# Kernel optimization log

Hardware: AMD Instinct MI355X
Metric: run time of the kernel (lower is better)

Reference implementation:

```python
import jax, jax.numpy as jnp
import numpy as np

B, Q, K, D, H, DH = 4, 512, 4096, 1024, 8, 128  # qk_channels=v_channels=out=1024

def setup_inputs() -> dict:
    key = jax.random.key(0)
    ks = jax.random.split(key, 5)
    s = 1.0 / np.sqrt(D)
    return {
        "inputs_q": jax.random.normal(ks[0], (B, Q, D), jnp.float32),
        "inputs_kv": jax.random.normal(ks[1], (B, K, D), jnp.float32),
        "Wq": jax.random.normal(ks[2], (D, H, DH), jnp.float32) * s,
        "Wkv": jax.random.normal(ks[3], (D, H, 2 * DH), jnp.float32) * s,
        "Wproj": jax.random.normal(ks[4], (H, DH, D), jnp.float32) * (1.0 / np.sqrt(H * DH)),
        "b_proj": jnp.zeros((D,), jnp.float32),
    }

def reference(inputs_q, inputs_kv, Wq, Wkv, Wproj, b_proj):
    # QKV projections (no bias)
    q = jnp.einsum('bqd,dhe->bqhe', inputs_q, Wq)          # [B,Q,H,DH]
    kv = jnp.einsum('bkd,dhe->bkhe', inputs_kv, Wkv)        # [B,K,H,2*DH]
    k, v = kv[..., :DH], kv[..., DH:]
    # scaled dot-product attention (softmax in fp32, per source)
    attn = jnp.einsum('bqhd,bkhd->bhqk', q, k) / np.sqrt(DH)
    attn = jax.nn.softmax(attn.astype(jnp.float32), axis=-1).astype(v.dtype)
    o = jnp.einsum('bhqk,bkhd->bqhd', attn, v)              # [B,Q,H,DH]
    # output projection contracting (head, head_dim), with bias
    return jnp.einsum('bqhd,hdo->bqo', o, Wproj) + b_proj   # [B,Q,D]
```

## Files before the change

### kernel.cpp

```cpp
#include <hip/hip_runtime.h>
#include <hip/hip_bf16.h>
#include <cstdint>

typedef unsigned short u16;
typedef unsigned int u32;
typedef __bf16 bf16x8 __attribute__((ext_vector_type(8)));
typedef u16 u16x8 __attribute__((ext_vector_type(8)));
typedef u16 u16x4 __attribute__((ext_vector_type(4)));
typedef float f32x4 __attribute__((ext_vector_type(4)));

#define MFMA16(a, b, c) __builtin_amdgcn_mfma_f32_16x16x32_bf16(a, b, c, 0, 0, 0)

__device__ __forceinline__ void async16(const void* g, void* s) {
    __builtin_amdgcn_global_load_lds((const __attribute__((address_space(1))) void*)g,
                                     (__attribute__((address_space(3))) void*)s, 16, 0, 0);
}

__device__ __forceinline__ u16 f2bf(float f) {
    u32 u; __builtin_memcpy(&u, &f, 4);
    u = u + 0x7fffu + ((u >> 16) & 1u);
    return (u16)(u >> 16);
}

__global__ __launch_bounds__(256) void prep_all(const float* __restrict__ inq,
                                                u16* __restrict__ Aq,
                                                const float* __restrict__ inkv,
                                                u16* __restrict__ Akv,
                                                const float* __restrict__ Wq,  u16* __restrict__ WqT,
                                                const float* __restrict__ Wkv, u16* __restrict__ WkvT,
                                                const float* __restrict__ Wp,  u16* __restrict__ WpT) {
    __shared__ u16 t[64][65];
    const int blk = blockIdx.x;
    const int tid = threadIdx.x;
    if (blk < 9216) {
        const float* in; u16* out; size_t i;
        if (blk < 1024) { in = inq;  out = Aq;  i = (size_t)blk * 256 + tid; }
        else            { in = inkv; out = Akv; i = (size_t)(blk - 1024) * 256 + tid; }
        const float4* p = (const float4*)in + i * 2;
        const float4 a = p[0], b = p[1];
        u16x8 v;
        v[0] = f2bf(a.x); v[1] = f2bf(a.y); v[2] = f2bf(a.z); v[3] = f2bf(a.w);
        v[4] = f2bf(b.x); v[5] = f2bf(b.y); v[6] = f2bf(b.z); v[7] = f2bf(b.w);
        ((u16x8*)out)[i] = v;
        return;
    }
    const int wblk = blk - 9216;
    const float* in; u16* out; int R, C, bx, by;
    if (wblk < 256)      { in = Wq;  out = WqT;  R = 1024; C = 1024; bx = wblk & 15;  by = wblk >> 4; }
    else if (wblk < 768) { in = Wkv; out = WkvT; R = 1024; C = 2048; bx = (wblk - 256) & 31; by = (wblk - 256) >> 5; }
    else                 { in = Wp;  out = WpT;  R = 1024; C = 1024; bx = (wblk - 768) & 15; by = (wblk - 768) >> 4; }
    const int r0 = by << 6, c0 = bx << 6;
#pragma unroll
    for (int i = 0; i < 16; i++) {
        int idx = i * 256 + tid;
        int r = idx >> 6, c = idx & 63;
        t[r][c] = f2bf(in[(size_t)(r0 + r) * C + c0 + c]);
    }
    __syncthreads();
#pragma unroll
    for (int i = 0; i < 16; i++) {
        int idx = i * 256 + tid;
        int c = idx >> 6, r = idx & 63;
        out[(size_t)(c0 + c) * R + r0 + r] = t[r][c];
    }
}

template <bool OUTF32, int NT>
__global__ __launch_bounds__(256) void gemm_bt(const u16* __restrict__ A,
                                               const u16* __restrict__ B,
                                               void* __restrict__ Cv,
                                               const float* __restrict__ bias,
                                               int M, int N, int K) {
    constexpr int NJ = NT / 32;
    __shared__ __align__(16) u16 As[128 * 64];
    __shared__ __align__(16) u16 Bs[NT * 64];
    const int tid = threadIdx.x;
    const int wave = tid >> 6, lane = tid & 63;
    const int lrow = lane & 15, quad = lane >> 4;
    const int nb = N / NT;
    const int bx = blockIdx.x % nb, by = blockIdx.x / nb;
    const long m0 = (long)by << 7, n0 = (long)bx * NT;
    const int wm = (wave >> 1) << 6, wn = (wave & 1) * (NT / 2);

    const f32x4 fz = {0.f, 0.f, 0.f, 0.f};
    f32x4 acc[4][NJ];
#pragma unroll
    for (int i = 0; i < 4; i++)
#pragma unroll
        for (int j = 0; j < NJ; j++) acc[i][j] = fz;

    const int srow = wave * 8 + (lane >> 3);
    const int scol = ((lane & 7) ^ (lane >> 3)) << 3;
    const u16* Ag = A + (m0 + srow) * K + scol;
    const u16* Bg = B + (n0 + srow) * K + scol;
    u16* AsW = &As[wave * 512];
    u16* BsW = &Bs[wave * 512];

    for (int k0 = 0; k0 < K; k0 += 64) {
        __syncthreads();
#pragma unroll
        for (int c = 0; c < 4; c++)
            async16(Ag + (long)c * 32 * K + k0, AsW + c * 2048);
#pragma unroll
        for (int c = 0; c < NT / 32; c++)
            async16(Bg + (long)c * 32 * K + k0, BsW + c * 2048);
        __syncthreads();
#pragma unroll
        for (int c = 0; c < 2; c++) {
            bf16x8 af[4], bfr[NJ];
#pragma unroll
            for (int i = 0; i < 4; i++) {
                const int row = wm + i * 16 + lrow;
                af[i] = *(const bf16x8*)&As[row * 64 + (((c * 4 + quad) ^ (row & 7)) << 3)];
            }
#pragma unroll
            for (int j = 0; j < NJ; j++) {
                const int row = wn + j * 16 + lrow;
                bfr[j] = *(const bf16x8*)&Bs[row * 64 + (((c * 4 + quad) ^ (row & 7)) << 3)];
            }
#pragma unroll
            for (int i = 0; i < 4; i++)
#pragma unroll
                for (int j = 0; j < NJ; j++)
                    acc[i][j] = MFMA16(bfr[j], af[i], acc[i][j]);
        }
    }
#pragma unroll
    for (int i = 0; i < 4; i++) {
        const long row = m0 + wm + i * 16 + lrow;
#pragma unroll
        for (int j = 0; j < NJ; j++) {
            const long colb = n0 + wn + j * 16 + quad * 4;
            if (OUTF32) {
                f32x4 v = acc[i][j];
                if (bias) v += *(const f32x4*)&bias[colb];
                *(f32x4*)&((float*)Cv)[row * N + colb] = v;
            } else {
                u16x4 pk;
#pragma unroll
                for (int r = 0; r < 4; r++) pk[r] = f2bf(acc[i][j][r]);
                *(u16x4*)&((u16*)Cv)[row * N + colb] = pk;
            }
        }
    }
}

__global__ __launch_bounds__(512, 2) void gemm_kv256(const u16* __restrict__ A,
                                                     const u16* __restrict__ B,
                                                     u16* __restrict__ C,
                                                     u16* __restrict__ Vt) {
    constexpr int K = 1024, N = 2048, NT = 16;
    __shared__ __align__(16) u16 As[2][256 * 64];
    __shared__ __align__(16) u16 Bs[2][256 * 64];
    const int tid = threadIdx.x;
    const int wave = tid >> 6, lane = tid & 63;
    const int lrow = lane & 15, quad = lane >> 4;
    const int wMi = wave >> 2, wNi = wave & 3;
    const int wm = wMi * 128, wn = wNi * 64;
    const int wg = blockIdx.x;
    const int swz = (wg & 7) * 64 + (wg >> 3);
    const int bx = swz & 7, by = swz >> 3;
    const long m0 = (long)by << 8, n0 = (long)bx << 8;

    const int srow = tid >> 3;
    const int scol = ((tid & 7) ^ (srow & 7)) << 3;
    const u16* Ag = A + (m0 + srow) * K + scol;
    const u16* Bg = B + (n0 + srow) * K + scol;
    const int sdst = tid * 8;

    auto stgA = [&](int bi, int h, int kt) {
        async16(Ag + (size_t)(h * 128) * K + kt * 64,      &As[bi][h * 8192 + sdst]);
        async16(Ag + (size_t)(h * 128 + 64) * K + kt * 64, &As[bi][h * 8192 + 4096 + sdst]);
    };
    auto stgB = [&](int bi, int h, int kt) {
        async16(Bg + (size_t)(h * 128) * K + kt * 64,      &Bs[bi][h * 8192 + sdst]);
        async16(Bg + (size_t)(h * 128 + 64) * K + kt * 64, &Bs[bi][h * 8192 + 4096 + sdst]);
    };

    stgB(0, 0, 0); stgB(0, 1, 0); stgA(0, 0, 0); stgA(0, 1, 0);
    stgB(1, 0, 1); stgB(1, 1, 1); stgA(1, 0, 1);

    const f32x4 fz = {0.f, 0.f, 0.f, 0.f};
    f32x4 acc[8][4];
#pragma unroll
    for (int i = 0; i < 8; i++)
#pragma unroll
        for (int j = 0; j < 4; j++) acc[i][j] = fz;

    asm volatile("s_waitcnt vmcnt(6)" ::: "memory");
    __builtin_amdgcn_s_barrier();

    bf16x8 av[4][2], bv[4][2];
    for (int t = 0; t < NT; ++t) {
        const int cur = t & 1, nxt = cur ^ 1;
#pragma unroll
        for (int i = 0; i < 4; i++) {
            const int row = wm + i * 16 + lrow;
#pragma unroll
            for (int c = 0; c < 2; c++)
                av[i][c] = *(const bf16x8*)&As[cur][row * 64 + (((c * 4 + quad) ^ (row & 7)) << 3)];
        }
#pragma unroll
        for (int j = 0; j < 4; j++) {
            const int row = wn + j * 16 + lrow;
#pragma unroll
            for (int c = 0; c < 2; c++)
                bv[j][c] = *(const bf16x8*)&Bs[cur][row * 64 + (((c * 4 + quad) ^ (row & 7)) << 3)];
        }
        if (t + 1 < NT) stgA(nxt, 1, t + 1);
        __builtin_amdgcn_s_barrier();
        asm volatile("s_waitcnt lgkmcnt(0)" ::: "memory");
        __builtin_amdgcn_sched_barrier(0);
        __builtin_amdgcn_s_setprio(1);
#pragma unroll
        for (int i = 0; i < 4; i++)
#pragma unroll
            for (int j = 0; j < 2; j++)
#pragma unroll
                for (int c = 0; c < 2; c++)
                    acc[i][j] = MFMA16(av[i][c], bv[j][c], acc[i][j]);
        __builtin_amdgcn_s_setprio(0);
        __builtin_amdgcn_s_barrier();
        if (t + 2 < NT) stgB(cur, 0, t + 2);
        __builtin_amdgcn_s_barrier();
        __builtin_amdgcn_sched_barrier(0);
        __builtin_amdgcn_s_setprio(1);
#pragma unroll
        for (int i = 0; i < 4; i++)
#pragma unroll
            for (int j = 2; j < 4; j++)
#pragma unroll
                for (int c = 0; c < 2; c++)
                    acc[i][j] = MFMA16(av[i][c], bv[j][c], acc[i][j]);
        __builtin_amdgcn_s_setprio(0);
        __builtin_amdgcn_s_barrier();
#pragma unroll
        for (int i = 0; i < 4; i++) {
            const int row = wm + (i + 4) * 16 + lrow;
#pragma unroll
            for (int c = 0; c < 2; c++)
                av[i][c] = *(const bf16x8*)&As[cur][row * 64 + (((c * 4 + quad) ^ (row & 7)) << 3)];
        }
        if (t + 2 < NT) stgB(cur, 1, t + 2);
        __builtin_amdgcn_s_barrier();
        asm volatile("s_waitcnt lgkmcnt(0)" ::: "memory");
        __builtin_amdgcn_sched_barrier(0);
        __builtin_amdgcn_s_setprio(1);
#pragma unroll
        for (int i = 0; i < 4; i++)
#pragma unroll
            for (int j = 0; j < 2; j++)
#pragma unroll
                for (int c = 0; c < 2; c++)
                    acc[i + 4][j] = MFMA16(av[i][c], bv[j][c], acc[i + 4][j]);
        __builtin_amdgcn_s_setprio(0);
        __builtin_amdgcn_s_barrier();
        if (t + 2 < NT) stgA(cur, 0, t + 2);
        __builtin_amdgcn_s_barrier();
        __builtin_amdgcn_sched_barrier(0);
        __builtin_amdgcn_s_setprio(1);
#pragma unroll
        for (int i = 0; i < 4; i++)
#pragma unroll
            for (int j = 2; j < 4; j++)
#pragma unroll
                for (int c = 0; c < 2; c++)
                    acc[i + 4][j] = MFMA16(av[i][c], bv[j][c], acc[i + 4][j]);
        __builtin_amdgcn_s_setprio(0);
        if (t + 2 < NT)      { asm volatile("s_waitcnt vmcnt(6)" ::: "memory"); }
        else if (t + 1 < NT) { asm volatile("s_waitcnt vmcnt(0)" ::: "memory"); }
        __builtin_amdgcn_s_barrier();
    }

    const int h = bx;
    if (wNi < 2) {
#pragma unroll
        for (int j = 0; j < 4; j++) {
            const long col = n0 + wn + j * 16 + lrow;
#pragma unroll
            for (int i = 0; i < 8; i++) {
                const long row = m0 + wm + i * 16 + quad * 4;
#pragma unroll
                for (int r = 0; r < 4; r++)
                    C[(row + r) * N + col] = f2bf(acc[i][j][r]);
            }
        }
    } else {
#pragma unroll
        for (int j = 0; j < 4; j++) {
            const int dh = (wNi - 2) * 64 + j * 16 + lrow;
#pragma unroll
            for (int i = 0; i < 8; i++) {
                const int row = (int)m0 + wm + i * 16 + quad * 4;
                const int b = row >> 12, kv = row & 4095;
                u16x4 pk;
#pragma unroll
                for (int r = 0; r < 4; r++) pk[r] = f2bf(acc[i][j][r]);
                *(u16x4*)&Vt[(((size_t)b * 8 + h) * 128 + dh) * 4096 + kv] = pk;
            }
        }
    }
}

__global__ __launch_bounds__(512, 4) void flash_attn_split(const u16* __restrict__ qb,
                                                           const u16* __restrict__ kvb,
                                                           const u16* __restrict__ vTb,
                                                           float* __restrict__ Opart,
                                                           float* __restrict__ Mpart,
                                                           float* __restrict__ Lpart) {
    __shared__ __align__(16) u16 Ks[2][64 * 128];
    __shared__ __align__(16) u16 Vs[2][128 * 64];
    __shared__ __align__(16) u16 Ps[8][16 * 64];
    const int tid = threadIdx.x, wave = tid >> 6, lane = tid & 63;
    const int lrow = lane & 15, quad = lane >> 4;
    const int p = blockIdx.x;
    const int blk = (p & 7) * 64 + (p >> 3);
    const int split = blk & 3, qt = (blk >> 2) & 3, h = (blk >> 4) & 7, b = blk >> 7;
    const int q0 = qt * 128;
    const int kbase = split * 1024;

    bf16x8 qf[4];
    {
        const u16* qp = qb + (((size_t)(b * 512 + q0 + wave * 16 + lrow) * 8 + h) << 7) + quad * 8;
#pragma unroll
        for (int c = 0; c < 4; c++) qf[c] = *(const bf16x8*)(qp + c * 32);
    }

    const f32x4 fz = {0.f, 0.f, 0.f, 0.f};
    f32x4 oacc[8];
#pragma unroll
    for (int g = 0; g < 8; g++) oacc[g] = fz;
    float mrow = -1e30f, lsum = 0.f;
    const float scale = 0.08838834764831845f;

    const int kRow = tid >> 4, kBlk = tid & 15;
    const int vRow = tid >> 3, vBlk = tid & 7;
    const u16* kg = kvb + (size_t)b * 4096 * 2048 + h * 256 + kBlk * 8;
    const u16* vg = vTb + (size_t)(b * 8 + h) * 128 * 4096 + vBlk * 8;
    const int ksw = (kBlk ^ (kRow & 15)) << 3;
    const int vsw = (vBlk ^ (vRow & 7)) << 3;

    {
        const bf16x8 a0 = *(const bf16x8*)&kg[(size_t)(kbase + kRow) * 2048];
        const bf16x8 a1 = *(const bf16x8*)&kg[(size_t)(kbase + 32 + kRow) * 2048];
        const bf16x8 b0 = *(const bf16x8*)&vg[(size_t)vRow * 4096 + kbase];
        const bf16x8 b1 = *(const bf16x8*)&vg[(size_t)(64 + vRow) * 4096 + kbase];
        *(bf16x8*)&Ks[0][kRow * 128 + ksw] = a0;
        *(bf16x8*)&Ks[0][(32 + kRow) * 128 + ksw] = a1;
        *(bf16x8*)&Vs[0][vRow * 64 + vsw] = b0;
        *(bf16x8*)&Vs[0][(64 + vRow) * 64 + vsw] = b1;
    }
    __syncthreads();

    for (int it = 0; it < 16; ++it) {
        const int cur = it & 1, nxt = cur ^ 1;
        const bool more = (it + 1 < 16);
        bf16x8 nk0, nk1, nv0, nv1;
        if (more) {
            const int k1 = kbase + (it + 1) * 64;
            nk0 = *(const bf16x8*)&kg[(size_t)(k1 + kRow) * 2048];
            nk1 = *(const bf16x8*)&kg[(size_t)(k1 + 32 + kRow) * 2048];
            nv0 = *(const bf16x8*)&vg[(size_t)vRow * 4096 + k1];
            nv1 = *(const bf16x8*)&vg[(size_t)(64 + vRow) * 4096 + k1];
        }

        f32x4 s[4];
        __builtin_amdgcn_s_setprio(1);
#pragma unroll
        for (int t = 0; t < 4; t++) {
            f32x4 a = fz;
#pragma unroll
            for (int c = 0; c < 4; c++) {
                const bf16x8 kf = *(const bf16x8*)
                    &Ks[cur][(t * 16 + lrow) * 128 + (((c * 4 + quad) ^ lrow) << 3)];
                a = MFMA16(kf, qf[c], a);
            }
            s[t] = a * scale;
        }
        __builtin_amdgcn_s_setprio(0);

        float mx = s[0][0];
#pragma unroll
        for (int t = 0; t < 4; t++)
#pragma unroll
            for (int r = 0; r < 4; r++) mx = fmaxf(mx, s[t][r]);
        mx = fmaxf(mx, __shfl_xor(mx, 16));
        mx = fmaxf(mx, __shfl_xor(mx, 32));
        float mn = fmaxf(mrow, mx);
        if (__all(mx <= mrow + 8.f)) {
            mn = mrow;
        } else {
            const float alpha = __expf(mrow - mn);
#pragma unroll
            for (int g = 0; g < 8; g++) oacc[g] *= alpha;
            lsum *= alpha;
            mrow = mn;
        }
        float sum = 0.f;
#pragma unroll
        for (int t = 0; t < 4; t++)
#pragma unroll
            for (int r = 0; r < 4; r++) {
                float pv = __expf(s[t][r] - mn);
                s[t][r] = pv;
                sum += pv;
            }
        sum += __shfl_xor(sum, 16);
        sum += __shfl_xor(sum, 32);
        lsum += sum;

        u16* Pw = &Ps[wave][0];
#pragma unroll
        for (int t = 0; t < 4; t++) {
            u16x4 pk;
#pragma unroll
            for (int r = 0; r < 4; r++) pk[r] = f2bf(s[t][r]);
            const int kvo = t * 16 + quad * 4;
            *(u16x4*)&Pw[lrow * 64 + (((kvo >> 3) ^ (lrow & 7)) << 3) + (kvo & 7)] = pk;
        }
        asm volatile("s_waitcnt lgkmcnt(0)" ::: "memory");
        __builtin_amdgcn_sched_barrier(0);
        const bf16x8 pf0 = *(const bf16x8*)&Pw[lrow * 64 + ((quad ^ (lrow & 7)) << 3)];
        const bf16x8 pf1 = *(const bf16x8*)&Pw[lrow * 64 + (((4 + quad) ^ (lrow & 7)) << 3)];

        __builtin_amdgcn_s_setprio(1);
#pragma unroll
        for (int g = 0; g < 8; g++) {
            f32x4 o = oacc[g];
            o = MFMA16(*(const bf16x8*)&Vs[cur][(g * 16 + lrow) * 64 + ((quad ^ (lrow & 7)) << 3)], pf0, o);
            o = MFMA16(*(const bf16x8*)&Vs[cur][(g * 16 + lrow) * 64 + (((4 + quad) ^ (lrow & 7)) << 3)], pf1, o);
            oacc[g] = o;
        }
        __builtin_amdgcn_s_setprio(0);

        if (more) {
            *(bf16x8*)&Ks[nxt][kRow * 128 + ksw] = nk0;
            *(bf16x8*)&Ks[nxt][(32 + kRow) * 128 + ksw] = nk1;
            *(bf16x8*)&Vs[nxt][vRow * 64 + vsw] = nv0;
            *(bf16x8*)&Vs[nxt][(64 + vRow) * 64 + vsw] = nv1;
        }
        __syncthreads();
    }

    float* Ob = Opart + (size_t)blk * 16384;
#pragma unroll
    for (int g = 0; g < 8; g++)
        *(f32x4*)&Ob[(wave * 16 + lrow) * 128 + g * 16 + quad * 4] = oacc[g];
    if (quad == 0) {
        const int row = blk * 128 + wave * 16 + lrow;
        Mpart[row] = mrow;
        Lpart[row] = lsum;
    }
}

__global__ __launch_bounds__(512) void combine_attn(const float* __restrict__ Opart,
                                                    const float* __restrict__ Mpart,
                                                    const float* __restrict__ Lpart,
                                                    u16* __restrict__ ob) {
    const int c = blockIdx.x;
    const int qt = c & 3, h = (c >> 2) & 7, b = c >> 5;
    const int lr = threadIdx.x >> 2, cg = (threadIdx.x & 3) * 32;
    float ms[4], w[4];
    float m = -1e30f;
#pragma unroll
    for (int s = 0; s < 4; s++) { ms[s] = Mpart[(c * 4 + s) * 128 + lr]; m = fmaxf(m, ms[s]); }
    float l = 0.f;
#pragma unroll
    for (int s = 0; s < 4; s++) { w[s] = __expf(ms[s] - m); l += w[s] * Lpart[(c * 4 + s) * 128 + lr]; }
    const float inv = 1.f / l;
#pragma unroll
    for (int s = 0; s < 4; s++) w[s] *= inv;
    const size_t orow = ((size_t)(b * 512 + qt * 128 + lr) * 8 + h) << 7;
#pragma unroll
    for (int j = 0; j < 4; j++) {
        f32x4 a0 = {0.f, 0.f, 0.f, 0.f}, a1 = a0;
#pragma unroll
        for (int s = 0; s < 4; s++) {
            const f32x4* pp = (const f32x4*)(Opart + ((size_t)(c * 4 + s)) * 16384 + (size_t)lr * 128 + cg + j * 8);
            a0 += pp[0] * w[s];
            a1 += pp[1] * w[s];
        }
        u16x8 v;
#pragma unroll
        for (int i = 0; i < 4; i++) { v[i] = f2bf(a0[i]); v[4 + i] = f2bf(a1[i]); }
        *(u16x8*)&ob[orow + cg + j * 8] = v;
    }
}

extern "C" void kernel_launch(void* const* d_in, const int* in_sizes, int n_in,
                              void* d_out, int out_size, void* d_ws, size_t ws_size,
                              hipStream_t stream) {
    const float* inq   = (const float*)d_in[0];
    const float* inkv  = (const float*)d_in[1];
    const float* Wq    = (const float*)d_in[2];
    const float* Wkv   = (const float*)d_in[3];
    const float* Wproj = (const float*)d_in[4];
    const float* bproj = (const float*)d_in[5];
    float* out = (float*)d_out;

    u16* WqT    = (u16*)d_ws;
    u16* WkvT   = WqT + (size_t)1024 * 1024;
    u16* WprojT = WkvT + (size_t)2048 * 1024;
    u16* Aq     = WprojT + (size_t)1024 * 1024;
    u16* Akv    = Aq + (size_t)2048 * 1024;
    u16* qbuf   = Akv + (size_t)16384 * 1024;
    u16* kvbuf  = qbuf + (size_t)2048 * 1024;
    u16* vTbuf  = kvbuf + (size_t)16384 * 2048;
    u16* obuf   = vTbuf + (size_t)32 * 128 * 4096;

    float* Opart = (float*)Akv;
    float* Mpart = (float*)Aq;
    float* Lpart = Mpart + 65536;

    prep_all<<<10240, 256, 0, stream>>>(inq, Aq, inkv, Akv, Wq, WqT, Wkv, WkvT, Wproj, WprojT);

    gemm_bt<false, 64><<<16 * 16, 256, 0, stream>>>(Aq, WqT, qbuf, nullptr, 2048, 1024, 1024);
    gemm_kv256<<<512, 512, 0, stream>>>(Akv, WkvT, kvbuf, vTbuf);

    flash_attn_split<<<512, 512, 0, stream>>>(qbuf, kvbuf, vTbuf, Opart, Mpart, Lpart);
    combine_attn<<<128, 512, 0, stream>>>(Opart, Mpart, Lpart, obuf);

    gemm_bt<true, 64><<<16 * 16, 256, 0, stream>>>(obuf, WprojT, (void*)out, bproj, 2048, 1024, 1024);
}
```

Before: 299.0 us.

## Merge Q projection GEMM into KV projection kernel launch as extra blocks

The separate Q-projection GEMM launch is removed. Its work is appended as 128 extra workgroups (128x128 tiles, two 4-wave teams each covering 64 columns) to the KV projection kernel, so both GEMMs share one launch. This removes a launch boundary and lets the Q tiles fill the tail of the KV grid. The Q path is a simple single-buffered loop with syncthreads, so it may be less efficient per tile than the old dedicated kernel.

```diff
diff --git a/kernel.cpp b/kernel.cpp
--- a/kernel.cpp
+++ b/kernel.cpp
@@ -145,20 +145,90 @@
     }
 }
 
-__global__ __launch_bounds__(512, 2) void gemm_kv256(const u16* __restrict__ A,
-                                                     const u16* __restrict__ B,
-                                                     u16* __restrict__ C,
-                                                     u16* __restrict__ Vt) {
+__global__ __launch_bounds__(512, 2) void gemm_kv_q(const u16* __restrict__ A,
+                                                    const u16* __restrict__ B,
+                                                    u16* __restrict__ C,
+                                                    u16* __restrict__ Vt,
+                                                    const u16* __restrict__ Aq,
+                                                    const u16* __restrict__ Wq,
+                                                    u16* __restrict__ qbuf) {
     constexpr int K = 1024, N = 2048, NT = 16;
     __shared__ __align__(16) u16 As[2][256 * 64];
     __shared__ __align__(16) u16 Bs[2][256 * 64];
     const int tid = threadIdx.x;
     const int wave = tid >> 6, lane = tid & 63;
     const int lrow = lane & 15, quad = lane >> 4;
+    const int p = blockIdx.x;
+    const f32x4 fz = {0.f, 0.f, 0.f, 0.f};
+
+    if (p >= 512) {
+        const int p2 = p - 512;
+        const int by = p2 >> 3, bxp = p2 & 7;
+        const long m0 = (long)by << 7, n0 = (long)bxp << 7;
+        constexpr int QN = 1024;
+        u16* qAs = &As[0][0];
+        u16* qBs = &Bs[0][0];
+        const int team = wave >> 2, wv = wave & 3;
+        const int wm = (wv >> 1) << 6, wn = (wv & 1) * 32;
+
+        f32x4 acc[4][2];
+#pragma unroll
+        for (int i = 0; i < 4; i++)
+#pragma unroll
+            for (int j = 0; j < 2; j++) acc[i][j] = fz;
+
+        const int srow = tid >> 3;
+        const int scol = ((tid & 7) ^ (srow & 7)) << 3;
+        const u16* Ag = Aq + (m0 + srow) * K + scol;
+        const u16* Bg = Wq + (n0 + srow) * K + scol;
+
+        for (int k0 = 0; k0 < K; k0 += 64) {
+            __syncthreads();
+#pragma unroll
+            for (int c = 0; c < 2; c++)
+                async16(Ag + (size_t)(c * 64) * K + k0, qAs + c * 4096 + tid * 8);
+#pragma unroll
+            for (int c = 0; c < 2; c++)
+                async16(Bg + (size_t)(c * 64) * K + k0, qBs + c * 4096 + tid * 8);
+            __syncthreads();
+#pragma unroll
+            for (int c = 0; c < 2; c++) {
+                bf16x8 af[4], bfr[2];
+#pragma unroll
+                for (int i = 0; i < 4; i++) {
+                    const int row = wm + i * 16 + lrow;
+                    af[i] = *(const bf16x8*)&qAs[row * 64 + (((c * 4 + quad) ^ (row & 7)) << 3)];
+                }
+#pragma unroll
+                for (int j = 0; j < 2; j++) {
+                    const int row = team * 64 + wn + j * 16 + lrow;
+                    bfr[j] = *(const bf16x8*)&qBs[row * 64 + (((c * 4 + quad) ^ (row & 7)) << 3)];
+                }
+#pragma unroll
+                for (int i = 0; i < 4; i++)
+#pragma unroll
+                    for (int j = 0; j < 2; j++)
+                        acc[i][j] = MFMA16(bfr[j], af[i], acc[i][j]);
+            }
+        }
+#pragma unroll
+        for (int i = 0; i < 4; i++) {
+            const long row = m0 + wm + i * 16 + lrow;
+#pragma unroll
+            for (int j = 0; j < 2; j++) {
+                const long colb = n0 + team * 64 + wn + j * 16 + quad * 4;
+                u16x4 pk;
+#pragma unroll
+                for (int r = 0; r < 4; r++) pk[r] = f2bf(acc[i][j][r]);
+                *(u16x4*)&qbuf[row * QN + colb] = pk;
+            }
+        }
+        return;
+    }
+
     const int wMi = wave >> 2, wNi = wave & 3;
     const int wm = wMi * 128, wn = wNi * 64;
-    const int wg = blockIdx.x;
-    const int swz = (wg & 7) * 64 + (wg >> 3);
+    const int swz = (p & 7) * 64 + (p >> 3);
     const int bx = swz & 7, by = swz >> 3;
     const long m0 = (long)by << 8, n0 = (long)bx << 8;
 
@@ -180,7 +250,6 @@
     stgB(0, 0, 0); stgB(0, 1, 0); stgA(0, 0, 0); stgA(0, 1, 0);
     stgB(1, 0, 1); stgB(1, 1, 1); stgA(1, 0, 1);
 
-    const f32x4 fz = {0.f, 0.f, 0.f, 0.f};
     f32x4 acc[8][4];
 #pragma unroll
     for (int i = 0; i < 8; i++)
@@ -514,8 +583,7 @@
 
     prep_all<<<10240, 256, 0, stream>>>(inq, Aq, inkv, Akv, Wq, WqT, Wkv, WkvT, Wproj, WprojT);
 
-    gemm_bt<false, 64><<<16 * 16, 256, 0, stream>>>(Aq, WqT, qbuf, nullptr, 2048, 1024, 1024);
-    gemm_kv256<<<512, 512, 0, stream>>>(Akv, WkvT, kvbuf, vTbuf);
+    gemm_kv_q<<<640, 512, 0, stream>>>(Akv, WkvT, kvbuf, vTbuf, Aq, WqT, qbuf);
 
     flash_attn_split<<<512, 512, 0, stream>>>(qbuf, kvbuf, vTbuf, Opart, Mpart, Lpart);
     combine_attn<<<128, 512, 0, stream>>>(Opart, Mpart, Lpart, obuf);
```

Result: no change. 301.8 us (+0.9%).

## Fuse split-KV combine into flash attention via last-block atomic counter

Applied to the files above, without the earlier changes.

Removes the separate combine_attn launch. Each split block now bumps a per-tile atomic counter after writing its partial results, and the last of the four splits merges the partial O, M and L into the bf16 output. Counters are zeroed inside prep_all. This saves one kernel launch and its tail, at the cost of threadfences and an atomic in every attention block, plus serialized combine work in the last-arriving blocks.

```diff
diff --git a/kernel.cpp b/kernel.cpp
--- a/kernel.cpp
+++ b/kernel.cpp
@@ -28,11 +28,13 @@
                                                 u16* __restrict__ Akv,
                                                 const float* __restrict__ Wq,  u16* __restrict__ WqT,
                                                 const float* __restrict__ Wkv, u16* __restrict__ WkvT,
-                                                const float* __restrict__ Wp,  u16* __restrict__ WpT) {
+                                                const float* __restrict__ Wp,  u16* __restrict__ WpT,
+                                                int* __restrict__ cnt) {
     __shared__ u16 t[64][65];
     const int blk = blockIdx.x;
     const int tid = threadIdx.x;
     if (blk < 9216) {
+        if (blk == 0 && tid < 128) cnt[tid] = 0;
         const float* in; u16* out; size_t i;
         if (blk < 1024) { in = inq;  out = Aq;  i = (size_t)blk * 256 + tid; }
         else            { in = inkv; out = Akv; i = (size_t)(blk - 1024) * 256 + tid; }
@@ -307,7 +309,9 @@
                                                            const u16* __restrict__ vTb,
                                                            float* __restrict__ Opart,
                                                            float* __restrict__ Mpart,
-                                                           float* __restrict__ Lpart) {
+                                                           float* __restrict__ Lpart,
+                                                           int* __restrict__ cnt,
+                                                           u16* __restrict__ ob) {
     __shared__ __align__(16) u16 Ks[2][64 * 128];
     __shared__ __align__(16) u16 Vs[2][128 * 64];
     __shared__ __align__(16) u16 Ps[8][16 * 64];
@@ -451,39 +455,42 @@
         Mpart[row] = mrow;
         Lpart[row] = lsum;
     }
-}
-
-__global__ __launch_bounds__(512) void combine_attn(const float* __restrict__ Opart,
-                                                    const float* __restrict__ Mpart,
-                                                    const float* __restrict__ Lpart,
-                                                    u16* __restrict__ ob) {
-    const int c = blockIdx.x;
-    const int qt = c & 3, h = (c >> 2) & 7, b = c >> 5;
-    const int lr = threadIdx.x >> 2, cg = (threadIdx.x & 3) * 32;
-    float ms[4], w[4];
-    float m = -1e30f;
-#pragma unroll
-    for (int s = 0; s < 4; s++) { ms[s] = Mpart[(c * 4 + s) * 128 + lr]; m = fmaxf(m, ms[s]); }
-    float l = 0.f;
-#pragma unroll
-    for (int s = 0; s < 4; s++) { w[s] = __expf(ms[s] - m); l += w[s] * Lpart[(c * 4 + s) * 128 + lr]; }
-    const float inv = 1.f / l;
-#pragma unroll
-    for (int s = 0; s < 4; s++) w[s] *= inv;
-    const size_t orow = ((size_t)(b * 512 + qt * 128 + lr) * 8 + h) << 7;
-#pragma unroll
-    for (int j = 0; j < 4; j++) {
-        f32x4 a0 = {0.f, 0.f, 0.f, 0.f}, a1 = a0;
-#pragma unroll
-        for (int s = 0; s < 4; s++) {
-            const f32x4* pp = (const f32x4*)(Opart + ((size_t)(c * 4 + s)) * 16384 + (size_t)lr * 128 + cg + j * 8);
-            a0 += pp[0] * w[s];
-            a1 += pp[1] * w[s];
-        }
-        u16x8 v;
-#pragma unroll
-        for (int i = 0; i < 4; i++) { v[i] = f2bf(a0[i]); v[4 + i] = f2bf(a1[i]); }
-        *(u16x8*)&ob[orow + cg + j * 8] = v;
+
+    __threadfence();
+    int* lastp = (int*)&Ks[0][0];
+    if (tid == 0) *lastp = (atomicAdd(&cnt[blk >> 2], 1) == 3) ? 1 : 0;
+    __syncthreads();
+    if (*lastp == 0) return;
+    __threadfence();
+    {
+        const int c = blk >> 2;
+        const int qt2 = c & 3, h2 = (c >> 2) & 7, b2 = c >> 5;
+        const int lr = tid >> 2, cg = (tid & 3) * 32;
+        float ms[4], w[4];
+        float m = -1e30f;
+#pragma unroll
+        for (int s = 0; s < 4; s++) { ms[s] = Mpart[(c * 4 + s) * 128 + lr]; m = fmaxf(m, ms[s]); }
+        float l = 0.f;
+#pragma unroll
+        for (int s = 0; s < 4; s++) { w[s] = __expf(ms[s] - m); l += w[s] * Lpart[(c * 4 + s) * 128 + lr]; }
+        const float inv = 1.f / l;
+#pragma unroll
+        for (int s = 0; s < 4; s++) w[s] *= inv;
+        const size_t orow = ((size_t)(b2 * 512 + qt2 * 128 + lr) * 8 + h2) << 7;
+#pragma unroll
+        for (int j = 0; j < 4; j++) {
+            f32x4 a0 = {0.f, 0.f, 0.f, 0.f}, a1 = a0;
+#pragma unroll
+            for (int s = 0; s < 4; s++) {
+                const f32x4* pp = (const f32x4*)(Opart + ((size_t)(c * 4 + s)) * 16384 + (size_t)lr * 128 + cg + j * 8);
+                a0 += pp[0] * w[s];
+                a1 += pp[1] * w[s];
+            }
+            u16x8 v;
+#pragma unroll
+            for (int i = 0; i < 4; i++) { v[i] = f2bf(a0[i]); v[4 + i] = f2bf(a1[i]); }
+            *(u16x8*)&ob[orow + cg + j * 8] = v;
+        }
     }
 }
 
@@ -507,18 +514,18 @@
     u16* kvbuf  = qbuf + (size_t)2048 * 1024;
     u16* vTbuf  = kvbuf + (size_t)16384 * 2048;
     u16* obuf   = vTbuf + (size_t)32 * 128 * 4096;
+    int* cnt    = (int*)(obuf + (size_t)2048 * 1024);
 
     float* Opart = (float*)Akv;
     float* Mpart = (float*)Aq;
     float* Lpart = Mpart + 65536;
 
-    prep_all<<<10240, 256, 0, stream>>>(inq, Aq, inkv, Akv, Wq, WqT, Wkv, WkvT, Wproj, WprojT);
+    prep_all<<<10240, 256, 0, stream>>>(inq, Aq, inkv, Akv, Wq, WqT, Wkv, WkvT, Wproj, WprojT, cnt);
 
     gemm_bt<false, 64><<<16 * 16, 256, 0, stream>>>(Aq, WqT, qbuf, nullptr, 2048, 1024, 1024);
     gemm_kv256<<<512, 512, 0, stream>>>(Akv, WkvT, kvbuf, vTbuf);
 
-    flash_attn_split<<<512, 512, 0, stream>>>(qbuf, kvbuf, vTbuf, Opart, Mpart, Lpart);
-    combine_attn<<<128, 512, 0, stream>>>(Opart, Mpart, Lpart, obuf);
+    flash_attn_split<<<512, 512, 0, stream>>>(qbuf, kvbuf, vTbuf, Opart, Mpart, Lpart, cnt, obuf);
 
     gemm_bt<true, 64><<<16 * 16, 256, 0, stream>>>(obuf, WprojT, (void*)out, bproj, 2048, 1024, 1024);
 }
```

New measurement: 454.3 us. 51.9% more time.
